# Optimization experiments

Measured on AMD Instinct MI355X. Metric: run time of the kernel, lower is better.

Reference implementation:

```python
import jax, jax.numpy as jnp
import numpy as np

SEQ_LEN = 4096
INPUT_SIZE = 1024
OUTPUT_SIZE = 1024


def _xavier(key, shape):
    n = shape[0]
    lim = 1.0 / (n ** 0.5)
    return jax.random.uniform(key, shape, minval=-lim, maxval=lim, dtype=jnp.float32)


def setup_inputs() -> dict:
    key = jax.random.key(0)
    kx, kk, kv, kq = jax.random.split(key, 4)
    X = jax.random.normal(kx, (SEQ_LEN, INPUT_SIZE), dtype=jnp.float32)
    Wk = _xavier(kk, (INPUT_SIZE, OUTPUT_SIZE))
    Wv = _xavier(kv, (INPUT_SIZE, OUTPUT_SIZE))
    Wq = _xavier(kq, (INPUT_SIZE, OUTPUT_SIZE))
    return {"X": X, "Wk": Wk, "Wv": Wv, "Wq": Wq}


def reference(X, Wk, Wv, Wq):
    # Faithful to original: scores = K @ Q^T (note K first, no 1/sqrt(d) scaling)
    K = X @ Wk  # (S, D)
    V = X @ Wv  # (S, D)
    Q = X @ Wq  # (S, D)
    scores = jnp.einsum('sd,td->st', K, Q)  # (S, S) == K @ Q^T
    attn = jax.nn.softmax(scores, axis=-1) @ V  # (S, D)
    return attn
```

## Files before the change

kernel.cpp:

```cpp
#include <hip/hip_runtime.h>
#include <hip/hip_fp16.h>
#include <cstdint>

#define SEQ 4096
#define DIM 1024

typedef _Float16 f16x8 __attribute__((ext_vector_type(8)));
typedef float f32x16 __attribute__((ext_vector_type(16)));
typedef __attribute__((address_space(1))) void as1_void;
typedef __attribute__((address_space(3))) void as3_void;

__device__ __forceinline__ ushort f2h(float f) {
  _Float16 h = (_Float16)f;
  return __builtin_bit_cast(ushort, h);
}

__global__ void convert_all_kernel(const float* __restrict__ X, const float* __restrict__ Wk,
                                   const float* __restrict__ Wv, const float* __restrict__ Wq,
                                   ushort* __restrict__ Xh, ushort* __restrict__ Wt) {
  const int z = blockIdx.z;
  const int tx = threadIdx.x, ty = threadIdx.y;
  if (z == 3) {
    const int bid = blockIdx.y * 32 + blockIdx.x;
    const int t = ty * 32 + tx;
#pragma unroll
    for (int k = 0; k < 4; k++) {
      int i = bid * 1024 + k * 256 + t;
      float4 v = reinterpret_cast<const float4*>(X)[i];
      ushort4 o = { f2h(v.x), f2h(v.y), f2h(v.z), f2h(v.w) };
      reinterpret_cast<ushort4*>(Xh)[i] = o;
    }
    return;
  }
  __shared__ float tile[32][33];
  const float* W = (z == 0) ? Wk : (z == 1) ? Wv : Wq;
  int n0 = blockIdx.x * 32, k0 = blockIdx.y * 32;
#pragma unroll
  for (int r = 0; r < 4; r++) {
    int k = ty + r * 8;
    tile[k][tx] = W[(size_t)(k0 + k) * DIM + n0 + tx];
  }
  __syncthreads();
  ushort* out = Wt + (size_t)z * DIM * DIM;
#pragma unroll
  for (int r = 0; r < 4; r++) {
    int n = ty + r * 8;
    out[(size_t)(n0 + n) * DIM + k0 + tx] = f2h(tile[tx][n]);
  }
}

__device__ __forceinline__ void gemm_tile256(const ushort* __restrict__ A,
                                             const ushort* __restrict__ B,
                                             ushort* __restrict__ C,
                                             int N, int K, int m0, int n0,
                                             int kt0, int ktend) {
  constexpr int BK = 64;
  __shared__ __align__(16) ushort As[2][256 * BK];
  __shared__ __align__(16) ushort Bs[2][256 * BK];
  const int tid = threadIdx.x;
  const int wave = tid >> 6, lane = tid & 63;
  const int l31 = lane & 31, khalf = lane >> 5;
  const int wm = (wave & 1) * 128, wn = (wave >> 1) * 64;

  const int srow = tid >> 3;
  const int skey = ((srow & 7) ^ ((srow >> 3) & 3));
  const int sce = (((tid & 7) ^ skey) * 8);
  const int rk = (l31 & 7) ^ ((l31 >> 3) & 3);

  f32x16 acc[4][2];
#pragma unroll
  for (int i = 0; i < 4; i++)
#pragma unroll
    for (int j = 0; j < 2; j++)
#pragma unroll
      for (int r = 0; r < 16; r++) acc[i][j][r] = 0.f;

  const ushort* Abase = A + (size_t)(m0 + srow) * K + sce;
  const ushort* Bbase = B + (size_t)(n0 + srow) * K + sce;
  const int ldsbase = wave * 512;

#pragma unroll
  for (int q = 0; q < 4; q++)
    __builtin_amdgcn_global_load_lds((const as1_void*)(Abase + (size_t)q * 64 * K + kt0),
                                     (as3_void*)&As[0][ldsbase + q * 4096], 16, 0, 0);
#pragma unroll
  for (int q = 0; q < 4; q++)
    __builtin_amdgcn_global_load_lds((const as1_void*)(Bbase + (size_t)q * 64 * K + kt0),
                                     (as3_void*)&Bs[0][ldsbase + q * 4096], 16, 0, 0);
  __syncthreads();

  const int ntiles = (ktend - kt0) >> 6;
  for (int tt = 0; tt < ntiles; ++tt) {
    const int cur = tt & 1;
    const int kt = kt0 + tt * BK;
    const bool pf = (tt + 1 < ntiles);
    const ushort* As_c = As[cur];
    const ushort* Bs_c = Bs[cur];
#pragma unroll
    for (int ks = 0; ks < 4; ks++) {
      f16x8 af[4], bf2[2];
      const int co = (((ks * 2 + khalf) ^ rk) * 8);
#pragma unroll
      for (int i = 0; i < 4; i++)
        af[i] = *reinterpret_cast<const f16x8*>(&As_c[(wm + i * 32 + l31) * BK + co]);
#pragma unroll
      for (int j = 0; j < 2; j++)
        bf2[j] = *reinterpret_cast<const f16x8*>(&Bs_c[(wn + j * 32 + l31) * BK + co]);
      if (pf && ks == 0) {
#pragma unroll
        for (int q = 0; q < 4; q++)
          __builtin_amdgcn_global_load_lds(
              (const as1_void*)(Abase + (size_t)q * 64 * K + kt + BK),
              (as3_void*)&As[cur ^ 1][ldsbase + q * 4096], 16, 0, 0);
      }
      if (pf && ks == 1) {
#pragma unroll
        for (int q = 0; q < 4; q++)
          __builtin_amdgcn_global_load_lds(
              (const as1_void*)(Bbase + (size_t)q * 64 * K + kt + BK),
              (as3_void*)&Bs[cur ^ 1][ldsbase + q * 4096], 16, 0, 0);
      }
      __builtin_amdgcn_s_barrier();
      __builtin_amdgcn_s_setprio(1);
#pragma unroll
      for (int i = 0; i < 4; i++)
#pragma unroll
        for (int j = 0; j < 2; j++)
          acc[i][j] = __builtin_amdgcn_mfma_f32_32x32x16_f16(af[i], bf2[j], acc[i][j], 0, 0, 0);
      __builtin_amdgcn_s_setprio(0);
      if (ks < 3) __builtin_amdgcn_s_barrier();
    }
    __syncthreads();
  }

#pragma unroll
  for (int i = 0; i < 4; i++)
#pragma unroll
    for (int j = 0; j < 2; j++)
#pragma unroll
      for (int r = 0; r < 16; r++) {
        int row = m0 + wm + i * 32 + (r & 3) + 8 * (r >> 2) + 4 * khalf;
        int col = n0 + wn + j * 32 + l31;
        C[(size_t)row * N + col] = f2h(acc[i][j][r]);
      }
}

__global__ __launch_bounds__(512, 2) void proj256_kernel(const ushort* __restrict__ Xh,
                                                         const ushort* __restrict__ Wt,
                                                         ushort* __restrict__ Kh,
                                                         ushort* __restrict__ Qh,
                                                         ushort* __restrict__ Vt) {
  const int b = blockIdx.x;
  const ushort* A;
  const ushort* B;
  ushort* Cp;
  int N, m0, n0;
  if (b < 128) {
    const int z = b >> 6, q = b & 63;
    A = Xh;
    B = Wt + (size_t)(z ? 2 : 0) * DIM * DIM;
    Cp = z ? Qh : Kh;
    N = DIM;
    m0 = (q >> 2) * 256;
    n0 = (q & 3) * 256;
  } else {
    const int q = b - 128;
    A = Wt + (size_t)DIM * DIM;
    B = Xh;
    Cp = Vt;
    N = SEQ;
    m0 = (q >> 4) * 256;
    n0 = (q & 15) * 256;
  }
  gemm_tile256(A, B, Cp, N, DIM, m0, n0, 0, DIM);
}

__global__ __launch_bounds__(512, 2) void score256_kernel(const ushort* __restrict__ Kh,
                                                          const ushort* __restrict__ Qh,
                                                          ushort* __restrict__ S) {
  const int f = blockIdx.x;
  const int t = (f & 7) * 32 + (f >> 3);
  gemm_tile256(Kh, Qh, S, SEQ, DIM, (t >> 4) * 256, (t & 15) * 256, 0, DIM);
}

__global__ __launch_bounds__(512, 2) void out256_kernel(const ushort* __restrict__ P,
                                                        const ushort* __restrict__ Vt,
                                                        ushort* __restrict__ Part) {
  const int f = blockIdx.x;
  const int z = f >> 6;
  const int q = f & 63;
  const int t = (q & 7) * 8 + (q >> 3);
  ushort* Cp = Part + (size_t)z * SEQ * DIM;
  gemm_tile256(P, Vt, Cp, DIM, SEQ, (t >> 2) * 256, (t & 3) * 256,
               z * (SEQ / 4), (z + 1) * (SEQ / 4));
}

__global__ void reduce4_kernel(const ushort* __restrict__ Part, float* __restrict__ out, int n8) {
  int i = blockIdx.x * blockDim.x + threadIdx.x;
  if (i >= n8) return;
  const f16x8* p0 = reinterpret_cast<const f16x8*>(Part);
  const f16x8* p1 = p0 + n8;
  const f16x8* p2 = p1 + n8;
  const f16x8* p3 = p2 + n8;
  f16x8 a = p0[i], b = p1[i], c = p2[i], d = p3[i];
  float4 lo, hi;
  lo.x = (float)a[0] + (float)b[0] + (float)c[0] + (float)d[0];
  lo.y = (float)a[1] + (float)b[1] + (float)c[1] + (float)d[1];
  lo.z = (float)a[2] + (float)b[2] + (float)c[2] + (float)d[2];
  lo.w = (float)a[3] + (float)b[3] + (float)c[3] + (float)d[3];
  hi.x = (float)a[4] + (float)b[4] + (float)c[4] + (float)d[4];
  hi.y = (float)a[5] + (float)b[5] + (float)c[5] + (float)d[5];
  hi.z = (float)a[6] + (float)b[6] + (float)c[6] + (float)d[6];
  hi.w = (float)a[7] + (float)b[7] + (float)c[7] + (float)d[7];
  reinterpret_cast<float4*>(out)[i * 2] = lo;
  reinterpret_cast<float4*>(out)[i * 2 + 1] = hi;
}

__global__ __launch_bounds__(256) void softmax_kernel(const ushort* __restrict__ S,
                                                      ushort* __restrict__ P) {
  const int wave = threadIdx.x >> 6, lane = threadIdx.x & 63;
  const int row = blockIdx.x * 4 + wave;
  const ushort* s = S + (size_t)row * SEQ;
  float v[64];
#pragma unroll
  for (int i = 0; i < 8; i++) {
    f16x8 h = reinterpret_cast<const f16x8*>(s)[i * 64 + lane];
#pragma unroll
    for (int j = 0; j < 8; j++) v[i * 8 + j] = (float)h[j];
  }
  float m = v[0];
#pragma unroll
  for (int j = 1; j < 64; j++) m = fmaxf(m, v[j]);
#pragma unroll
  for (int o = 32; o > 0; o >>= 1) m = fmaxf(m, __shfl_xor(m, o, 64));
  float sum = 0.f;
#pragma unroll
  for (int j = 0; j < 64; j++) {
    v[j] = __expf(v[j] - m);
    sum += v[j];
  }
#pragma unroll
  for (int o = 32; o > 0; o >>= 1) sum += __shfl_xor(sum, o, 64);
  float inv = 1.0f / sum;
  ushort* p = P + (size_t)row * SEQ;
#pragma unroll
  for (int i = 0; i < 8; i++) {
    f16x8 h;
#pragma unroll
    for (int j = 0; j < 8; j++) h[j] = (_Float16)(v[i * 8 + j] * inv);
    reinterpret_cast<f16x8*>(p)[i * 64 + lane] = h;
  }
}

extern "C" void kernel_launch(void* const* d_in, const int* in_sizes, int n_in,
                              void* d_out, int out_size, void* d_ws, size_t ws_size,
                              hipStream_t stream) {
  const float* X = (const float*)d_in[0];
  const float* Wk = (const float*)d_in[1];
  const float* Wv = (const float*)d_in[2];
  const float* Wq = (const float*)d_in[3];

  char* ws = (char*)d_ws;
  size_t off = 0;
  ushort* Xh = (ushort*)(ws + off); off += (size_t)SEQ * DIM * 2;
  ushort* Wt = (ushort*)(ws + off); off += (size_t)3 * DIM * DIM * 2;
  ushort* Kh = (ushort*)(ws + off); off += (size_t)SEQ * DIM * 2;
  ushort* Qh = (ushort*)(ws + off); off += (size_t)SEQ * DIM * 2;
  ushort* Vt = (ushort*)(ws + off); off += (size_t)SEQ * DIM * 2;
  ushort* S = (ushort*)(ws + off);  off += (size_t)SEQ * SEQ * 2;
  ushort* P = (ushort*)(ws + off);  off += (size_t)SEQ * SEQ * 2;

  ushort* Part = S;

  convert_all_kernel<<<dim3(32, 32, 4), dim3(32, 8), 0, stream>>>(X, Wk, Wv, Wq, Xh, Wt);
  proj256_kernel<<<256, 512, 0, stream>>>(Xh, Wt, Kh, Qh, Vt);
  score256_kernel<<<256, 512, 0, stream>>>(Kh, Qh, S);
  softmax_kernel<<<1024, 256, 0, stream>>>(S, P);
  out256_kernel<<<256, 512, 0, stream>>>(P, Vt, Part);
  reduce4_kernel<<<SEQ * DIM / 8 / 256, 256, 0, stream>>>(Part, (float*)d_out, SEQ * DIM / 8);
}
```

Baseline: 208.1 us.

## Prefetch two K-tiles ahead with vmcnt-based waits in GEMM loop

Restructures the GEMM main loop so two tiles are issued up front and each iteration refills the buffer just consumed. Completion is tracked with explicit s_waitcnt vmcnt(8) instead of a full __syncthreads, and the per-k-step trailing barriers are removed. This is meant to keep a full tile of loads in flight during compute and cut barrier overhead. It risks races: with only two buffers, the new load into the current buffer is issued after one barrier, so correctness depends on every wave having finished its LDS reads before that barrier.

```diff
diff --git a/kernel.cpp b/kernel.cpp
--- a/kernel.cpp
+++ b/kernel.cpp
@@ -79,21 +79,26 @@
   const ushort* Bbase = B + (size_t)(n0 + srow) * K + sce;
   const int ldsbase = wave * 512;
 
-#pragma unroll
-  for (int q = 0; q < 4; q++)
-    __builtin_amdgcn_global_load_lds((const as1_void*)(Abase + (size_t)q * 64 * K + kt0),
-                                     (as3_void*)&As[0][ldsbase + q * 4096], 16, 0, 0);
-#pragma unroll
-  for (int q = 0; q < 4; q++)
-    __builtin_amdgcn_global_load_lds((const as1_void*)(Bbase + (size_t)q * 64 * K + kt0),
-                                     (as3_void*)&Bs[0][ldsbase + q * 4096], 16, 0, 0);
-  __syncthreads();
+  auto stage = [&](int buf, int kt) {
+#pragma unroll
+    for (int q = 0; q < 4; q++)
+      __builtin_amdgcn_global_load_lds((const as1_void*)(Abase + (size_t)q * 64 * K + kt),
+                                       (as3_void*)&As[buf][ldsbase + q * 4096], 16, 0, 0);
+#pragma unroll
+    for (int q = 0; q < 4; q++)
+      __builtin_amdgcn_global_load_lds((const as1_void*)(Bbase + (size_t)q * 64 * K + kt),
+                                       (as3_void*)&Bs[buf][ldsbase + q * 4096], 16, 0, 0);
+  };
 
   const int ntiles = (ktend - kt0) >> 6;
+
+  stage(0, kt0);
+  stage(1, kt0 + BK);
+  asm volatile("s_waitcnt vmcnt(8)" ::: "memory");
+  __builtin_amdgcn_s_barrier();
+
   for (int tt = 0; tt < ntiles; ++tt) {
     const int cur = tt & 1;
-    const int kt = kt0 + tt * BK;
-    const bool pf = (tt + 1 < ntiles);
     const ushort* As_c = As[cur];
     const ushort* Bs_c = Bs[cur];
 #pragma unroll
@@ -106,20 +111,6 @@
 #pragma unroll
       for (int j = 0; j < 2; j++)
         bf2[j] = *reinterpret_cast<const f16x8*>(&Bs_c[(wn + j * 32 + l31) * BK + co]);
-      if (pf && ks == 0) {
-#pragma unroll
-        for (int q = 0; q < 4; q++)
-          __builtin_amdgcn_global_load_lds(
-              (const as1_void*)(Abase + (size_t)q * 64 * K + kt + BK),
-              (as3_void*)&As[cur ^ 1][ldsbase + q * 4096], 16, 0, 0);
-      }
-      if (pf && ks == 1) {
-#pragma unroll
-        for (int q = 0; q < 4; q++)
-          __builtin_amdgcn_global_load_lds(
-              (const as1_void*)(Bbase + (size_t)q * 64 * K + kt + BK),
-              (as3_void*)&Bs[cur ^ 1][ldsbase + q * 4096], 16, 0, 0);
-      }
       __builtin_amdgcn_s_barrier();
       __builtin_amdgcn_s_setprio(1);
 #pragma unroll
@@ -128,9 +119,16 @@
         for (int j = 0; j < 2; j++)
           acc[i][j] = __builtin_amdgcn_mfma_f32_32x32x16_f16(af[i], bf2[j], acc[i][j], 0, 0, 0);
       __builtin_amdgcn_s_setprio(0);
-      if (ks < 3) __builtin_amdgcn_s_barrier();
     }
-    __syncthreads();
+    __builtin_amdgcn_s_barrier();
+    if (tt + 2 < ntiles) {
+      stage(cur, kt0 + (tt + 2) * BK);
+      asm volatile("s_waitcnt vmcnt(8)" ::: "memory");
+      __builtin_amdgcn_s_barrier();
+    } else if (tt + 1 < ntiles) {
+      asm volatile("s_waitcnt vmcnt(0)" ::: "memory");
+      __builtin_amdgcn_s_barrier();
+    }
   }
 
 #pragma unroll
```

After: 213.6 us. 2.7% more time.

## Restructure GEMM main loop into quadrant-wise ping-pong with split prefetches

Applied to the files above, without the earlier changes.

Reorganizes the K-tile loop so each wave loads full-K fragments for one 64x32 quadrant at a time and runs MFMAs per quadrant, instead of iterating over four k-steps with all fragments. The global-to-LDS prefetches for the next tile are split into four chunks, one per quadrant phase, so loads interleave with MFMA bursts. The end-of-tile __syncthreads is replaced by an explicit vmcnt wait plus s_barrier that is skipped on the last tile. The intent is better overlap of LDS reads, global loads and MFMA work with less full synchronization. The cost is a larger fragment register footprint and extra barriers per tile, which could hurt occupancy.

```diff
diff --git a/kernel.cpp b/kernel.cpp
--- a/kernel.cpp
+++ b/kernel.cpp
@@ -79,6 +79,8 @@
   const ushort* Bbase = B + (size_t)(n0 + srow) * K + sce;
   const int ldsbase = wave * 512;
 
+  const int ntiles = (ktend - kt0) >> 6;
+
 #pragma unroll
   for (int q = 0; q < 4; q++)
     __builtin_amdgcn_global_load_lds((const as1_void*)(Abase + (size_t)q * 64 * K + kt0),
@@ -87,50 +89,113 @@
   for (int q = 0; q < 4; q++)
     __builtin_amdgcn_global_load_lds((const as1_void*)(Bbase + (size_t)q * 64 * K + kt0),
                                      (as3_void*)&Bs[0][ldsbase + q * 4096], 16, 0, 0);
-  __syncthreads();
-
-  const int ntiles = (ktend - kt0) >> 6;
+  asm volatile("s_waitcnt vmcnt(0)" ::: "memory");
+  __builtin_amdgcn_s_barrier();
+
   for (int tt = 0; tt < ntiles; ++tt) {
-    const int cur = tt & 1;
-    const int kt = kt0 + tt * BK;
+    const int cur = tt & 1, nb = cur ^ 1;
+    const int nkt = kt0 + (tt + 1) * BK;
     const bool pf = (tt + 1 < ntiles);
     const ushort* As_c = As[cur];
     const ushort* Bs_c = Bs[cur];
-#pragma unroll
-    for (int ks = 0; ks < 4; ks++) {
-      f16x8 af[4], bf2[2];
-      const int co = (((ks * 2 + khalf) ^ rk) * 8);
-#pragma unroll
-      for (int i = 0; i < 4; i++)
-        af[i] = *reinterpret_cast<const f16x8*>(&As_c[(wm + i * 32 + l31) * BK + co]);
-#pragma unroll
-      for (int j = 0; j < 2; j++)
-        bf2[j] = *reinterpret_cast<const f16x8*>(&Bs_c[(wn + j * 32 + l31) * BK + co]);
-      if (pf && ks == 0) {
-#pragma unroll
-        for (int q = 0; q < 4; q++)
-          __builtin_amdgcn_global_load_lds(
-              (const as1_void*)(Abase + (size_t)q * 64 * K + kt + BK),
-              (as3_void*)&As[cur ^ 1][ldsbase + q * 4096], 16, 0, 0);
-      }
-      if (pf && ks == 1) {
-#pragma unroll
-        for (int q = 0; q < 4; q++)
-          __builtin_amdgcn_global_load_lds(
-              (const as1_void*)(Bbase + (size_t)q * 64 * K + kt + BK),
-              (as3_void*)&Bs[cur ^ 1][ldsbase + q * 4096], 16, 0, 0);
-      }
+
+    f16x8 af[2][4];
+    f16x8 bf[4];
+
+#pragma unroll
+    for (int mi = 0; mi < 2; mi++)
+#pragma unroll
+      for (int k = 0; k < 4; k++)
+        af[mi][k] = *reinterpret_cast<const f16x8*>(
+            &As_c[(wm + mi * 32 + l31) * BK + ((((k * 2 + khalf)) ^ rk) * 8)]);
+#pragma unroll
+    for (int k = 0; k < 4; k++)
+      bf[k] = *reinterpret_cast<const f16x8*>(
+          &Bs_c[(wn + l31) * BK + ((((k * 2 + khalf)) ^ rk) * 8)]);
+    if (pf) {
+#pragma unroll
+      for (int q = 0; q < 2; q++)
+        __builtin_amdgcn_global_load_lds((const as1_void*)(Abase + (size_t)q * 64 * K + nkt),
+                                         (as3_void*)&As[nb][ldsbase + q * 4096], 16, 0, 0);
+    }
+    __builtin_amdgcn_s_barrier();
+    __builtin_amdgcn_s_setprio(1);
+#pragma unroll
+    for (int k = 0; k < 4; k++)
+#pragma unroll
+      for (int mi = 0; mi < 2; mi++)
+        acc[mi][0] = __builtin_amdgcn_mfma_f32_32x32x16_f16(af[mi][k], bf[k], acc[mi][0], 0, 0, 0);
+    __builtin_amdgcn_s_setprio(0);
+    __builtin_amdgcn_s_barrier();
+
+#pragma unroll
+    for (int mi = 0; mi < 2; mi++)
+#pragma unroll
+      for (int k = 0; k < 4; k++)
+        af[mi][k] = *reinterpret_cast<const f16x8*>(
+            &As_c[(wm + 64 + mi * 32 + l31) * BK + ((((k * 2 + khalf)) ^ rk) * 8)]);
+    if (pf) {
+#pragma unroll
+      for (int q = 2; q < 4; q++)
+        __builtin_amdgcn_global_load_lds((const as1_void*)(Abase + (size_t)q * 64 * K + nkt),
+                                         (as3_void*)&As[nb][ldsbase + q * 4096], 16, 0, 0);
+    }
+    __builtin_amdgcn_s_barrier();
+    __builtin_amdgcn_s_setprio(1);
+#pragma unroll
+    for (int k = 0; k < 4; k++)
+#pragma unroll
+      for (int mi = 0; mi < 2; mi++)
+        acc[2 + mi][0] = __builtin_amdgcn_mfma_f32_32x32x16_f16(af[mi][k], bf[k], acc[2 + mi][0], 0, 0, 0);
+    __builtin_amdgcn_s_setprio(0);
+    __builtin_amdgcn_s_barrier();
+
+#pragma unroll
+    for (int k = 0; k < 4; k++)
+      bf[k] = *reinterpret_cast<const f16x8*>(
+          &Bs_c[(wn + 32 + l31) * BK + ((((k * 2 + khalf)) ^ rk) * 8)]);
+    if (pf) {
+#pragma unroll
+      for (int q = 0; q < 2; q++)
+        __builtin_amdgcn_global_load_lds((const as1_void*)(Bbase + (size_t)q * 64 * K + nkt),
+                                         (as3_void*)&Bs[nb][ldsbase + q * 4096], 16, 0, 0);
+    }
+    __builtin_amdgcn_s_barrier();
+    __builtin_amdgcn_s_setprio(1);
+#pragma unroll
+    for (int k = 0; k < 4; k++)
+#pragma unroll
+      for (int mi = 0; mi < 2; mi++)
+        acc[2 + mi][1] = __builtin_amdgcn_mfma_f32_32x32x16_f16(af[mi][k], bf[k], acc[2 + mi][1], 0, 0, 0);
+    __builtin_amdgcn_s_setprio(0);
+    __builtin_amdgcn_s_barrier();
+
+#pragma unroll
+    for (int mi = 0; mi < 2; mi++)
+#pragma unroll
+      for (int k = 0; k < 4; k++)
+        af[mi][k] = *reinterpret_cast<const f16x8*>(
+            &As_c[(wm + mi * 32 + l31) * BK + ((((k * 2 + khalf)) ^ rk) * 8)]);
+    if (pf) {
+#pragma unroll
+      for (int q = 2; q < 4; q++)
+        __builtin_amdgcn_global_load_lds((const as1_void*)(Bbase + (size_t)q * 64 * K + nkt),
+                                         (as3_void*)&Bs[nb][ldsbase + q * 4096], 16, 0, 0);
+    }
+    __builtin_amdgcn_s_barrier();
+    __builtin_amdgcn_s_setprio(1);
+#pragma unroll
+    for (int k = 0; k < 4; k++)
+#pragma unroll
+      for (int mi = 0; mi < 2; mi++)
+        acc[mi][1] = __builtin_amdgcn_mfma_f32_32x32x16_f16(af[mi][k], bf[k], acc[mi][1], 0, 0, 0);
+    __builtin_amdgcn_s_setprio(0);
+    __builtin_amdgcn_s_barrier();
+
+    if (pf) {
+      asm volatile("s_waitcnt vmcnt(0)" ::: "memory");
       __builtin_amdgcn_s_barrier();
-      __builtin_amdgcn_s_setprio(1);
-#pragma unroll
-      for (int i = 0; i < 4; i++)
-#pragma unroll
-        for (int j = 0; j < 2; j++)
-          acc[i][j] = __builtin_amdgcn_mfma_f32_32x32x16_f16(af[i], bf2[j], acc[i][j], 0, 0, 0);
-      __builtin_amdgcn_s_setprio(0);
-      if (ks < 3) __builtin_amdgcn_s_barrier();
-    }
-    __syncthreads();
+    }
   }
 
 #pragma unroll
```

Result: slower. 217.2 us (+4.4%).

## Fuse softmax into score epilogue stats and PV GEMM prologue

Applied to the files above, without the earlier changes.

The score GEMM epilogue now computes per-tile row max and sum-of-exp and writes them to a stats buffer that reuses the Xh region. The PV GEMM combines the 16 partial stats per row, loads raw scores through registers, applies exp and normalization, and writes the result to LDS, so the standalone softmax kernel and its 32MB write of P are gone. In exchange the A operand is no longer loaded asynchronously into LDS, and exp work is redone inside the GEMM loop, which adds register pressure and may stall the pipeline.

```diff
diff --git a/kernel.cpp b/kernel.cpp
--- a/kernel.cpp
+++ b/kernel.cpp
@@ -7,12 +7,16 @@
 
 typedef _Float16 f16x8 __attribute__((ext_vector_type(8)));
 typedef float f32x16 __attribute__((ext_vector_type(16)));
+typedef ushort u16x8 __attribute__((ext_vector_type(8)));
 typedef __attribute__((address_space(1))) void as1_void;
 typedef __attribute__((address_space(3))) void as3_void;
 
 __device__ __forceinline__ ushort f2h(float f) {
   _Float16 h = (_Float16)f;
   return __builtin_bit_cast(ushort, h);
+}
+__device__ __forceinline__ float h2f(ushort u) {
+  return (float)__builtin_bit_cast(_Float16, u);
 }
 
 __global__ void convert_all_kernel(const float* __restrict__ X, const float* __restrict__ Wk,
@@ -49,11 +53,13 @@
   }
 }
 
+template <bool STATS>
 __device__ __forceinline__ void gemm_tile256(const ushort* __restrict__ A,
                                              const ushort* __restrict__ B,
                                              ushort* __restrict__ C,
                                              int N, int K, int m0, int n0,
-                                             int kt0, int ktend) {
+                                             int kt0, int ktend,
+                                             float2* __restrict__ Stats, int cb) {
   constexpr int BK = 64;
   __shared__ __align__(16) ushort As[2][256 * BK];
   __shared__ __align__(16) ushort Bs[2][256 * BK];
@@ -79,6 +85,8 @@
   const ushort* Bbase = B + (size_t)(n0 + srow) * K + sce;
   const int ldsbase = wave * 512;
 
+  const int ntiles = (ktend - kt0) >> 6;
+
 #pragma unroll
   for (int q = 0; q < 4; q++)
     __builtin_amdgcn_global_load_lds((const as1_void*)(Abase + (size_t)q * 64 * K + kt0),
@@ -89,17 +97,16 @@
                                      (as3_void*)&Bs[0][ldsbase + q * 4096], 16, 0, 0);
   __syncthreads();
 
-  const int ntiles = (ktend - kt0) >> 6;
   for (int tt = 0; tt < ntiles; ++tt) {
-    const int cur = tt & 1;
-    const int kt = kt0 + tt * BK;
+    const int cur = tt & 1, nb = cur ^ 1;
+    const int nkt = kt0 + (tt + 1) * BK;
     const bool pf = (tt + 1 < ntiles);
     const ushort* As_c = As[cur];
     const ushort* Bs_c = Bs[cur];
 #pragma unroll
     for (int ks = 0; ks < 4; ks++) {
       f16x8 af[4], bf2[2];
-      const int co = (((ks * 2 + khalf) ^ rk) * 8);
+      const int co = (((ks * 2 + khalf)) ^ rk) * 8;
 #pragma unroll
       for (int i = 0; i < 4; i++)
         af[i] = *reinterpret_cast<const f16x8*>(&As_c[(wm + i * 32 + l31) * BK + co]);
@@ -109,19 +116,19 @@
       if (pf && ks == 0) {
 #pragma unroll
         for (int q = 0; q < 4; q++)
-          __builtin_amdgcn_global_load_lds(
-              (const as1_void*)(Abase + (size_t)q * 64 * K + kt + BK),
-              (as3_void*)&As[cur ^ 1][ldsbase + q * 4096], 16, 0, 0);
+          __builtin_amdgcn_global_load_lds((const as1_void*)(Abase + (size_t)q * 64 * K + nkt),
+                                           (as3_void*)&As[nb][ldsbase + q * 4096], 16, 0, 0);
       }
       if (pf && ks == 1) {
 #pragma unroll
         for (int q = 0; q < 4; q++)
-          __builtin_amdgcn_global_load_lds(
-              (const as1_void*)(Bbase + (size_t)q * 64 * K + kt + BK),
-              (as3_void*)&Bs[cur ^ 1][ldsbase + q * 4096], 16, 0, 0);
+          __builtin_amdgcn_global_load_lds((const as1_void*)(Bbase + (size_t)q * 64 * K + nkt),
+                                           (as3_void*)&Bs[nb][ldsbase + q * 4096], 16, 0, 0);
       }
       __builtin_amdgcn_s_barrier();
       __builtin_amdgcn_s_setprio(1);
+#pragma unroll
+      for (int k = 0; k < 4; k++) { (void)k; }
 #pragma unroll
       for (int i = 0; i < 4; i++)
 #pragma unroll
@@ -143,6 +150,52 @@
         int col = n0 + wn + j * 32 + l31;
         C[(size_t)row * N + col] = f2h(acc[i][j][r]);
       }
+
+  if constexpr (STATS) {
+    float* sm = reinterpret_cast<float*>(&As[0][0]);
+    const int wcol = wave >> 1;
+    __syncthreads();
+#pragma unroll
+    for (int i = 0; i < 4; i++)
+#pragma unroll
+      for (int r = 0; r < 16; r++) {
+        float a0 = h2f(f2h(acc[i][0][r]));
+        float a1 = h2f(f2h(acc[i][1][r]));
+        float mx = fmaxf(a0, a1);
+#pragma unroll
+        for (int o = 16; o > 0; o >>= 1) mx = fmaxf(mx, __shfl_xor(mx, o, 64));
+        if (l31 == 0) {
+          int rowl = wm + i * 32 + (r & 3) + 8 * (r >> 2) + 4 * khalf;
+          sm[rowl * 4 + wcol] = mx;
+        }
+      }
+    __syncthreads();
+    if (tid < 256) {
+      float rm = fmaxf(fmaxf(sm[tid * 4], sm[tid * 4 + 1]),
+                       fmaxf(sm[tid * 4 + 2], sm[tid * 4 + 3]));
+      sm[2048 + tid] = rm;
+    }
+    __syncthreads();
+#pragma unroll
+    for (int i = 0; i < 4; i++)
+#pragma unroll
+      for (int r = 0; r < 16; r++) {
+        int rowl = wm + i * 32 + (r & 3) + 8 * (r >> 2) + 4 * khalf;
+        float rm = sm[2048 + rowl];
+        float a0 = h2f(f2h(acc[i][0][r]));
+        float a1 = h2f(f2h(acc[i][1][r]));
+        float s = __expf(a0 - rm) + __expf(a1 - rm);
+#pragma unroll
+        for (int o = 16; o > 0; o >>= 1) s += __shfl_xor(s, o, 64);
+        if (l31 == 0) sm[1024 + rowl * 4 + wcol] = s;
+      }
+    __syncthreads();
+    if (tid < 256) {
+      float sum = sm[1024 + tid * 4] + sm[1024 + tid * 4 + 1] +
+                  sm[1024 + tid * 4 + 2] + sm[1024 + tid * 4 + 3];
+      Stats[(size_t)cb * SEQ + m0 + tid] = make_float2(sm[2048 + tid], sum);
+    }
+  }
 }
 
 __global__ __launch_bounds__(512, 2) void proj256_kernel(const ushort* __restrict__ Xh,
@@ -172,27 +225,161 @@
     m0 = (q >> 4) * 256;
     n0 = (q & 15) * 256;
   }
-  gemm_tile256(A, B, Cp, N, DIM, m0, n0, 0, DIM);
+  gemm_tile256<false>(A, B, Cp, N, DIM, m0, n0, 0, DIM, nullptr, 0);
 }
 
 __global__ __launch_bounds__(512, 2) void score256_kernel(const ushort* __restrict__ Kh,
                                                           const ushort* __restrict__ Qh,
-                                                          ushort* __restrict__ S) {
+                                                          ushort* __restrict__ S,
+                                                          float2* __restrict__ Stats) {
   const int f = blockIdx.x;
   const int t = (f & 7) * 32 + (f >> 3);
-  gemm_tile256(Kh, Qh, S, SEQ, DIM, (t >> 4) * 256, (t & 15) * 256, 0, DIM);
-}
-
-__global__ __launch_bounds__(512, 2) void out256_kernel(const ushort* __restrict__ P,
-                                                        const ushort* __restrict__ Vt,
-                                                        ushort* __restrict__ Part) {
+  const int ty = t >> 4, tx = t & 15;
+  gemm_tile256<true>(Kh, Qh, S, SEQ, DIM, ty * 256, tx * 256, 0, DIM, Stats, tx);
+}
+
+__global__ __launch_bounds__(512, 2) void out_sm256_kernel(const ushort* __restrict__ S,
+                                                           const ushort* __restrict__ Vt,
+                                                           const float2* __restrict__ Stats,
+                                                           ushort* __restrict__ Part) {
+  constexpr int BK = 64;
+  __shared__ __align__(16) ushort As[2][256 * BK];
+  __shared__ __align__(16) ushort Bs[2][256 * BK];
+  __shared__ float rowm[256], rowinv[256];
+
   const int f = blockIdx.x;
   const int z = f >> 6;
-  const int q = f & 63;
-  const int t = (q & 7) * 8 + (q >> 3);
-  ushort* Cp = Part + (size_t)z * SEQ * DIM;
-  gemm_tile256(P, Vt, Cp, DIM, SEQ, (t >> 2) * 256, (t & 3) * 256,
-               z * (SEQ / 4), (z + 1) * (SEQ / 4));
+  const int q0 = f & 63;
+  const int t = (q0 & 7) * 8 + (q0 >> 3);
+  const int m0 = (t >> 2) * 256, n0 = (t & 3) * 256;
+  const int kt0 = z * (SEQ / 4);
+  const int K = SEQ, N = DIM;
+  ushort* C = Part + (size_t)z * SEQ * DIM;
+
+  const int tid = threadIdx.x;
+  const int wave = tid >> 6, lane = tid & 63;
+  const int l31 = lane & 31, khalf = lane >> 5;
+  const int wm = (wave & 1) * 128, wn = (wave >> 1) * 64;
+
+  const int srow = tid >> 3;
+  const int skey = ((srow & 7) ^ ((srow >> 3) & 3));
+  const int sce = (((tid & 7) ^ skey) * 8);
+  const int rk = (l31 & 7) ^ ((l31 >> 3) & 3);
+
+  if (tid < 256) {
+    float mg = -3.4e38f;
+#pragma unroll
+    for (int cb = 0; cb < 16; cb++)
+      mg = fmaxf(mg, Stats[(size_t)cb * SEQ + m0 + tid].x);
+    float sg = 0.f;
+#pragma unroll
+    for (int cb = 0; cb < 16; cb++) {
+      float2 st = Stats[(size_t)cb * SEQ + m0 + tid];
+      sg += st.y * __expf(st.x - mg);
+    }
+    rowm[tid] = mg;
+    rowinv[tid] = 1.0f / sg;
+  }
+
+  f32x16 acc[4][2];
+#pragma unroll
+  for (int i = 0; i < 4; i++)
+#pragma unroll
+    for (int j = 0; j < 2; j++)
+#pragma unroll
+      for (int r = 0; r < 16; r++) acc[i][j][r] = 0.f;
+
+  const ushort* Abase = S + (size_t)(m0 + srow) * K + sce;
+  const ushort* Bbase = Vt + (size_t)(n0 + srow) * K + sce;
+  const int ldsbase = wave * 512;
+  const int ntiles = (SEQ / 4) >> 6;
+
+  u16x8 areg[4];
+#pragma unroll
+  for (int q = 0; q < 4; q++)
+    areg[q] = *reinterpret_cast<const u16x8*>(Abase + (size_t)q * 64 * K + kt0);
+#pragma unroll
+  for (int q = 0; q < 4; q++)
+    __builtin_amdgcn_global_load_lds((const as1_void*)(Bbase + (size_t)q * 64 * K + kt0),
+                                     (as3_void*)&Bs[0][ldsbase + q * 4096], 16, 0, 0);
+  __syncthreads();
+
+  float rm_[4], ri_[4];
+#pragma unroll
+  for (int q = 0; q < 4; q++) {
+    rm_[q] = rowm[srow + q * 64];
+    ri_[q] = rowinv[srow + q * 64];
+  }
+#pragma unroll
+  for (int q = 0; q < 4; q++) {
+    u16x8 o;
+#pragma unroll
+    for (int k2 = 0; k2 < 8; k2++)
+      o[k2] = f2h(__expf(h2f(areg[q][k2]) - rm_[q]) * ri_[q]);
+    *reinterpret_cast<u16x8*>(&As[0][ldsbase + q * 4096 + (lane & 63) * 8]) = o;
+  }
+  __syncthreads();
+
+  for (int tt = 0; tt < ntiles; ++tt) {
+    const int cur = tt & 1, nb = cur ^ 1;
+    const int nkt = kt0 + (tt + 1) * BK;
+    const bool pf = (tt + 1 < ntiles);
+    const ushort* As_c = As[cur];
+    const ushort* Bs_c = Bs[cur];
+#pragma unroll
+    for (int ks = 0; ks < 4; ks++) {
+      f16x8 af[4], bf2[2];
+      const int co = (((ks * 2 + khalf)) ^ rk) * 8;
+#pragma unroll
+      for (int i = 0; i < 4; i++)
+        af[i] = *reinterpret_cast<const f16x8*>(&As_c[(wm + i * 32 + l31) * BK + co]);
+#pragma unroll
+      for (int j = 0; j < 2; j++)
+        bf2[j] = *reinterpret_cast<const f16x8*>(&Bs_c[(wn + j * 32 + l31) * BK + co]);
+      if (pf && ks == 0) {
+#pragma unroll
+        for (int q = 0; q < 4; q++)
+          areg[q] = *reinterpret_cast<const u16x8*>(Abase + (size_t)q * 64 * K + nkt);
+      }
+      if (pf && ks == 1) {
+#pragma unroll
+        for (int q = 0; q < 4; q++)
+          __builtin_amdgcn_global_load_lds((const as1_void*)(Bbase + (size_t)q * 64 * K + nkt),
+                                           (as3_void*)&Bs[nb][ldsbase + q * 4096], 16, 0, 0);
+      }
+      __builtin_amdgcn_s_barrier();
+      __builtin_amdgcn_s_setprio(1);
+#pragma unroll
+      for (int i = 0; i < 4; i++)
+#pragma unroll
+        for (int j = 0; j < 2; j++)
+          acc[i][j] = __builtin_amdgcn_mfma_f32_32x32x16_f16(af[i], bf2[j], acc[i][j], 0, 0, 0);
+      __builtin_amdgcn_s_setprio(0);
+      if (ks < 3) __builtin_amdgcn_s_barrier();
+    }
+    if (pf) {
+#pragma unroll
+      for (int q = 0; q < 4; q++) {
+        u16x8 o;
+#pragma unroll
+        for (int k2 = 0; k2 < 8; k2++)
+          o[k2] = f2h(__expf(h2f(areg[q][k2]) - rm_[q]) * ri_[q]);
+        *reinterpret_cast<u16x8*>(&As[nb][ldsbase + q * 4096 + (lane & 63) * 8]) = o;
+      }
+    }
+    __syncthreads();
+  }
+
+#pragma unroll
+  for (int i = 0; i < 4; i++)
+#pragma unroll
+    for (int j = 0; j < 2; j++)
+#pragma unroll
+      for (int r = 0; r < 16; r++) {
+        int row = m0 + wm + i * 32 + (r & 3) + 8 * (r >> 2) + 4 * khalf;
+        int col = n0 + wn + j * 32 + l31;
+        C[(size_t)row * N + col] = f2h(acc[i][j][r]);
+      }
 }
 
 __global__ void reduce4_kernel(const ushort* __restrict__ Part, float* __restrict__ out, int n8) {
@@ -216,42 +403,6 @@
   reinterpret_cast<float4*>(out)[i * 2 + 1] = hi;
 }
 
-__global__ __launch_bounds__(256) void softmax_kernel(const ushort* __restrict__ S,
-                                                      ushort* __restrict__ P) {
-  const int wave = threadIdx.x >> 6, lane = threadIdx.x & 63;
-  const int row = blockIdx.x * 4 + wave;
-  const ushort* s = S + (size_t)row * SEQ;
-  float v[64];
-#pragma unroll
-  for (int i = 0; i < 8; i++) {
-    f16x8 h = reinterpret_cast<const f16x8*>(s)[i * 64 + lane];
-#pragma unroll
-    for (int j = 0; j < 8; j++) v[i * 8 + j] = (float)h[j];
-  }
-  float m = v[0];
-#pragma unroll
-  for (int j = 1; j < 64; j++) m = fmaxf(m, v[j]);
-#pragma unroll
-  for (int o = 32; o > 0; o >>= 1) m = fmaxf(m, __shfl_xor(m, o, 64));
-  float sum = 0.f;
-#pragma unroll
-  for (int j = 0; j < 64; j++) {
-    v[j] = __expf(v[j] - m);
-    sum += v[j];
-  }
-#pragma unroll
-  for (int o = 32; o > 0; o >>= 1) sum += __shfl_xor(sum, o, 64);
-  float inv = 1.0f / sum;
-  ushort* p = P + (size_t)row * SEQ;
-#pragma unroll
-  for (int i = 0; i < 8; i++) {
-    f16x8 h;
-#pragma unroll
-    for (int j = 0; j < 8; j++) h[j] = (_Float16)(v[i * 8 + j] * inv);
-    reinterpret_cast<f16x8*>(p)[i * 64 + lane] = h;
-  }
-}
-
 extern "C" void kernel_launch(void* const* d_in, const int* in_sizes, int n_in,
                               void* d_out, int out_size, void* d_ws, size_t ws_size,
                               hipStream_t stream) {
@@ -270,12 +421,12 @@
   ushort* S = (ushort*)(ws + off);  off += (size_t)SEQ * SEQ * 2;
   ushort* P = (ushort*)(ws + off);  off += (size_t)SEQ * SEQ * 2;
 
-  ushort* Part = S;
+  float2* Stats = (float2*)Xh;
+  ushort* Part = P;
 
   convert_all_kernel<<<dim3(32, 32, 4), dim3(32, 8), 0, stream>>>(X, Wk, Wv, Wq, Xh, Wt);
   proj256_kernel<<<256, 512, 0, stream>>>(Xh, Wt, Kh, Qh, Vt);
-  score256_kernel<<<256, 512, 0, stream>>>(Kh, Qh, S);
-  softmax_kernel<<<1024, 256, 0, stream>>>(S, P);
-  out256_kernel<<<256, 512, 0, stream>>>(P, Vt, Part);
+  score256_kernel<<<256, 512, 0, stream>>>(Kh, Qh, S, Stats);
+  out_sm256_kernel<<<256, 512, 0, stream>>>(S, Vt, Stats, Part);
   reduce4_kernel<<<SEQ * DIM / 8 / 256, 256, 0, stream>>>(Part, (float*)d_out, SEQ * DIM / 8);
 }
```

New measurement: 241.0 us. 15.8% more time.
